# Kernel optimization log

Hardware: AMD Instinct MI355X
Metric: run time of the kernel (lower is better)

The kernel has to match this reference:

```python
import jax, jax.numpy as jnp
import numpy as np

T, D = 1024, 2048
H, KH, HD = 16, 4, 128
E, K, I = 8, 2, 2048
EPS = 1e-5
CAP = 30.0          # attn logit softcap and router logit softcap
BASE = 10000.0      # rope theta


def setup_inputs() -> dict:
    key = jax.random.key(0)
    ks = jax.random.split(key, 8)
    s = 0.02
    return {
        "positions": jnp.arange(T, dtype=jnp.int32),
        "hidden_states": jax.random.normal(ks[0], (T, D), jnp.float32),
        "w_qkv": jax.random.normal(ks[1], (D, (H + 2 * KH) * HD), jnp.float32) * s,
        "w_o": jax.random.normal(ks[2], (H * HD, D), jnp.float32) * s,
        "w_gate": jax.random.normal(ks[3], (D, E), jnp.float32) * s,
        "w_gate_up": jax.random.normal(ks[4], (E, D, 2 * I), jnp.float32) * s,
        "w_down": jax.random.normal(ks[5], (E, I, D), jnp.float32) * s,
        "w_pre_attn": 1.0 + 0.01 * jax.random.normal(ks[6], (D,), jnp.float32),
        "w_post_attn": jnp.ones((D,), jnp.float32),
        "w_pre_moe": 1.0 + 0.01 * jax.random.normal(ks[7], (D,), jnp.float32),
        "w_post_moe": jnp.ones((D,), jnp.float32),
    }


def rmsnorm(x, w):
    v = jnp.mean(jnp.square(x), axis=-1, keepdims=True)
    return x * jax.lax.rsqrt(v + EPS) * w


def rope_neox(pos, x):
    # x: [T, nH, HD]; full-head-dim neox-style rotation
    half = HD // 2
    inv = 1.0 / (BASE ** (jnp.arange(half, dtype=jnp.float32) * 2.0 / HD))
    f = pos.astype(jnp.float32)[:, None] * inv            # [T, half]
    cos, sin = jnp.cos(f)[:, None, :], jnp.sin(f)[:, None, :]
    x1, x2 = x[..., :half], x[..., half:]
    return jnp.concatenate([x1 * cos - x2 * sin, x2 * cos + x1 * sin], axis=-1)


def attention(pos, x, w_qkv, w_o):
    qkv = x @ w_qkv
    q, k, v = jnp.split(qkv, [H * HD, (H + KH) * HD], axis=-1)
    q = rope_neox(pos, q.reshape(T, H, HD))
    k = rope_neox(pos, k.reshape(T, KH, HD))
    v = v.reshape(T, KH, HD)
    rep = H // KH                                          # GQA repeat
    k = jnp.repeat(k, rep, axis=1)
    v = jnp.repeat(v, rep, axis=1)
    s = jnp.einsum('qhd,khd->hqk', q, k) * (HD ** -0.5)
    s = CAP * jnp.tanh(s / CAP)                            # tanh logit cap
    causal = pos[:, None] >= pos[None, :]
    s = jnp.where(causal[None], s, -1e30)
    p = jax.nn.softmax(s, axis=-1)
    o = jnp.einsum('hqk,khd->qhd', p, v).reshape(T, H * HD)
    return o @ w_o


def moe(x, w_gate, w_gate_up, w_down):
    logits = x @ w_gate
    logits = CAP * jnp.tanh(logits / CAP)                  # router softcap
    probs = jax.nn.softmax(logits, axis=-1)
    topv, topi = jax.lax.top_k(probs, K)                   # no renorm (Grok1)
    comb = jnp.zeros((T, E), probs.dtype).at[jnp.arange(T)[:, None], topi].set(topv)
    gu = jnp.einsum('td,edf->etf', x, w_gate_up)           # [E,T,2I]
    g, u = jnp.split(gu, 2, axis=-1)
    act = jax.nn.gelu(g, approximate=True) * u             # GeluAndMul(tanh)
    out_e = jnp.einsum('eti,eid->etd', act, w_down)        # [E,T,D]
    return jnp.einsum('etd,te->td', out_e, comb)


def reference(positions, hidden_states, w_qkv, w_o, w_gate, w_gate_up, w_down,
              w_pre_attn, w_post_attn, w_pre_moe, w_post_moe):
    resid = hidden_states
    h = rmsnorm(hidden_states, w_pre_attn)
    a = attention(positions, h, w_qkv, w_o)
    resid = resid + rmsnorm(a, w_post_attn)                # post_attn_norm + add
    h = rmsnorm(resid, w_pre_moe)
    m = moe(h, w_gate, w_gate_up, w_down)
    return resid + rmsnorm(m, w_post_moe)
```

## Files before the change

### kernel.cpp

```cpp
#include <hip/hip_runtime.h>

#define TT 1024
#define DD 2048
#define NH 16
#define NKV 4
#define HDIM 128
#define NE 8
#define NI 2048
#define EPSF 1e-5f
#define NP 4

typedef short bf16x8 __attribute__((ext_vector_type(8)));
typedef float f32x4 __attribute__((ext_vector_type(4)));

__device__ __forceinline__ unsigned short f2bf(float x) {
  unsigned u = __float_as_uint(x);
  u += 0x7FFFu + ((u >> 16) & 1u);
  return (unsigned short)(u >> 16);
}
__device__ __forceinline__ float bf2f(unsigned short h) {
  return __uint_as_float((unsigned)h << 16);
}
__device__ __forceinline__ void split2(float a, unsigned short& h,
                                       unsigned short& l) {
  h = f2bf(a);
  l = f2bf(a - bf2f(h));
}
__device__ __forceinline__ float tanh_cap30(float v) {
  float e = __expf(v * (2.f / 30.f));
  return 30.f - 60.f / (e + 1.f);
}

__device__ __forceinline__ float wave_sum(float v) {
#pragma unroll
  for (int m = 32; m >= 1; m >>= 1) v += __shfl_xor(v, m, 64);
  return v;
}

__device__ __forceinline__ int swz4(int r) { return (r ^ (r >> 2)) & 3; }
__device__ __forceinline__ int swz8(int r) { return (r ^ (r >> 3)) & 7; }

__device__ __forceinline__ int swzoff(int row, int k) {
  return (k & ~31) | ((((k >> 3) & 3) ^ swz4(row & 15)) << 3) | (k & 7);
}

__device__ __forceinline__ void stage_gll(const unsigned short* src, int ld,
                                          char* ldsbase, int wid, int lane) {
#pragma unroll
  for (int j = 0; j < 2; ++j) {
    int idx = (wid * 2 + j) * 64 + lane;
    int r = idx >> 2, c = idx & 3;
    const unsigned short* g = src + (long)r * ld + c * 8;
    __builtin_amdgcn_global_load_lds(
        (const __attribute__((address_space(1))) unsigned int*)g,
        (__attribute__((address_space(3))) unsigned int*)(ldsbase +
                                                         (wid * 2 + j) * 1024),
        16, 0, 0);
  }
}
__device__ __forceinline__ void ld_frag(const char* base, int wrow, int l15,
                                        int lg, bf16x8* dst) {
#pragma unroll
  for (int i = 0; i < 4; ++i) {
    int row = wrow + i * 16 + l15;
    dst[i] = *(const bf16x8*)(base + row * 64 + ((lg ^ swz4(row)) << 4));
  }
}
__device__ __forceinline__ void mm16(const bf16x8* xa, const bf16x8* xb,
                                     f32x4 (*acc)[4]) {
#pragma unroll
  for (int mi = 0; mi < 4; ++mi)
#pragma unroll
    for (int ni = 0; ni < 4; ++ni)
      acc[mi][ni] = __builtin_amdgcn_mfma_f32_16x16x32_bf16(
          xa[mi], xb[ni], acc[mi][ni], 0, 0, 0);
}

template <int MODE>
__global__ __launch_bounds__(256) void pgemm3_k(
    const unsigned short* __restrict__ Ah, const unsigned short* __restrict__ Al,
    const unsigned short* __restrict__ Bh, const unsigned short* __restrict__ Bl,
    float* __restrict__ C, int Kh, int lda, int ldb, int ldc, long czs,
    float escale, float* __restrict__ SM, float* __restrict__ SS,
    const float* __restrict__ Sf) {
  int z = blockIdx.z;
  int m0 = blockIdx.y * 128, n0 = blockIdx.x * 128;
  int k0 = 0, kend = Kh;
  const float* Sbase = nullptr;
  int head = 0;
  if (MODE == 0) {
    k0 = z * Kh;
    kend = k0 + Kh;
    C += (long)z * czs;
  } else if (MODE == 1) {
    if (blockIdx.x > blockIdx.y) return;
    Ah += (long)z * TT * lda;
    Al += (long)z * TT * lda;
    Bh += (long)(z >> 2) * TT * ldb;
    Bl += (long)(z >> 2) * TT * ldb;
    C += (long)z * czs;
  } else {
    head = z >> 3;
    int ch = z & 7;
    int limit = (blockIdx.y + 1) * 128;
    k0 = ch * 128;
    if (k0 >= limit) return;
    kend = k0 + 128;
    Sbase = Sf + (long)head * TT * TT;
    Bh += (long)(head >> 2) * HDIM * ldb;
    Bl += (long)(head >> 2) * HDIM * ldb;
    C += (long)ch * czs + head * HDIM;
  }

  __shared__ __align__(16) char lds[32768];
  __shared__ float mrow[128], invrow[128];
  int tid = threadIdx.x, lane = tid & 63, wid = tid >> 6;
  int wm = (wid >> 1) * 64, wn = (wid & 1) * 64;
  int l15 = lane & 15, lg = lane >> 4;

  if (MODE == 2) {
    if (tid < 128) {
      int q = m0 + tid;
      int nt = blockIdx.y + 1;
      float m = -1e30f;
      for (int t = 0; t < nt; ++t)
        m = fmaxf(m, SM[((long)head * 8 + t) * TT + q]);
      float den = 0.f;
      for (int t = 0; t < nt; ++t) {
        long so = ((long)head * 8 + t) * TT + q;
        den += SS[so] * __expf(SM[so] - m);
      }
      mrow[tid] = m;
      invrow[tid] = 1.f / den;
    }
  }

  f32x4 acc[4][4];
#pragma unroll
  for (int i = 0; i < 4; ++i)
#pragma unroll
    for (int j = 0; j < 4; ++j) acc[i][j] = {0.f, 0.f, 0.f, 0.f};

  for (int kt = k0; kt < kend; kt += 32) {
    __syncthreads();
    if (MODE == 2) {
#pragma unroll
      for (int j = 0; j < 2; ++j) {
        int idx = tid + j * 256;
        int r = idx >> 2, c = idx & 3;
        int q = m0 + r;
        const float* sp = Sbase + (long)q * TT + kt + c * 8;
        float4 s0 = *(const float4*)sp;
        float4 s1 = *(const float4*)(sp + 4);
        float mq = mrow[r], iq = invrow[r];
        bf16x8 ph, pl;
        int kg0 = kt + c * 8;
#pragma unroll
        for (int u = 0; u < 8; ++u) {
          float s = (u < 4) ? ((const float*)&s0)[u] : ((const float*)&s1)[u - 4];
          float p = (kg0 + u <= q) ? __expf(s - mq) * iq : 0.f;
          unsigned short hh, ll;
          split2(p, hh, ll);
          ((unsigned short*)&ph)[u] = hh;
          ((unsigned short*)&pl)[u] = ll;
        }
        int off = r * 64 + ((c ^ swz4(r)) << 4);
        *(bf16x8*)(lds + off) = ph;
        *(bf16x8*)(lds + 8192 + off) = pl;
      }
    } else {
      stage_gll(Ah + (long)m0 * lda + kt, lda, lds, wid, lane);
      stage_gll(Al + (long)m0 * lda + kt, lda, lds + 8192, wid, lane);
    }
    stage_gll(Bh + (long)n0 * ldb + kt, ldb, lds + 16384, wid, lane);
    stage_gll(Bl + (long)n0 * ldb + kt, ldb, lds + 24576, wid, lane);
    __syncthreads();
    bf16x8 fah[4], fal[4], fbh[4], fbl[4];
    ld_frag(lds, wm, l15, lg, fah);
    ld_frag(lds + 16384, wn, l15, lg, fbh);
    mm16(fah, fbh, acc);
    ld_frag(lds + 24576, wn, l15, lg, fbl);
    mm16(fah, fbl, acc);
    ld_frag(lds + 8192, wm, l15, lg, fal);
    mm16(fal, fbh, acc);
  }

  if (MODE == 1) {
    int bx = blockIdx.x;
    bool diag = (bx == blockIdx.y);
    float vcap[4][4][4];
#pragma unroll
    for (int mi = 0; mi < 4; ++mi)
#pragma unroll
      for (int ni = 0; ni < 4; ++ni)
#pragma unroll
        for (int rr = 0; rr < 4; ++rr)
          vcap[mi][ni][rr] = tanh_cap30(acc[mi][ni][rr] * escale);
#pragma unroll
    for (int mi = 0; mi < 4; ++mi)
#pragma unroll
      for (int ni = 0; ni < 4; ++ni)
#pragma unroll
        for (int rr = 0; rr < 4; ++rr) {
          int ml = m0 + wm + mi * 16 + lg * 4 + rr;
          int col = n0 + wn + ni * 16 + l15;
          C[(long)ml * ldc + col] = vcap[mi][ni][rr];
        }
    __syncthreads();
    float* wmx = (float*)lds;
    float* wsm = (float*)(lds + 1024);
    int ch = wid & 1;
#pragma unroll
    for (int mi = 0; mi < 4; ++mi)
#pragma unroll
      for (int rr = 0; rr < 4; ++rr) {
        int wr = wm + mi * 16 + lg * 4 + rr;
        int rowg = m0 + wr;
        float mx = -1e30f;
#pragma unroll
        for (int ni = 0; ni < 4; ++ni) {
          int colg = n0 + wn + ni * 16 + l15;
          if (!diag || colg <= rowg) mx = fmaxf(mx, vcap[mi][ni][rr]);
        }
#pragma unroll
        for (int mk = 1; mk <= 8; mk <<= 1)
          mx = fmaxf(mx, __shfl_xor(mx, mk, 64));
        if (l15 == 0) wmx[ch * 128 + wr] = mx;
      }
    __syncthreads();
#pragma unroll
    for (int mi = 0; mi < 4; ++mi)
#pragma unroll
      for (int rr = 0; rr < 4; ++rr) {
        int wr = wm + mi * 16 + lg * 4 + rr;
        int rowg = m0 + wr;
        float m2 = fmaxf(wmx[wr], wmx[128 + wr]);
        float s = 0.f;
#pragma unroll
        for (int ni = 0; ni < 4; ++ni) {
          int colg = n0 + wn + ni * 16 + l15;
          if (!diag || colg <= rowg) s += __expf(vcap[mi][ni][rr] - m2);
        }
#pragma unroll
        for (int mk = 1; mk <= 8; mk <<= 1) s += __shfl_xor(s, mk, 64);
        if (l15 == 0) wsm[ch * 128 + wr] = s;
      }
    __syncthreads();
    if (tid < 128) {
      float m2 = fmaxf(wmx[tid], wmx[128 + tid]);
      float s = wsm[tid] + wsm[128 + tid];
      long so = ((long)z * 8 + bx) * TT + m0 + tid;
      SM[so] = m2;
      SS[so] = s;
    }
    return;
  }

#pragma unroll
  for (int mi = 0; mi < 4; ++mi)
#pragma unroll
    for (int ni = 0; ni < 4; ++ni)
#pragma unroll
      for (int rr = 0; rr < 4; ++rr) {
        int ml = m0 + wm + mi * 16 + lg * 4 + rr;
        int col = n0 + wn + ni * 16 + l15;
        C[(long)ml * ldc + col] = acc[mi][ni][rr];
      }
}

template <int AMODE, int EP>
__global__ __launch_bounds__(256) void gemm_k(
    const unsigned short* __restrict__ A, const float* __restrict__ Bf,
    unsigned short* __restrict__ Cb, int N, int K, int lda, int ldb, int ldc,
    long bzs, long pzs, const int* __restrict__ cnt,
    const int* __restrict__ basep, const int* __restrict__ tok,
    const int* __restrict__ slotp, const float* __restrict__ wtp,
    unsigned short* __restrict__ slots_out) {
  int z = blockIdx.z;
  int e = z >> 1, kp = z & 1;
  Bf += (long)e * bzs;
  int Me = cnt[e], be = basep[e];
  int m0 = blockIdx.y * 128, n0 = blockIdx.x * 128;
  if (m0 >= Me) return;
  int Kc = K >> 1, kbeg = kp * Kc, klim = kbeg + Kc;

  __shared__ __align__(16) char lds[32768];
  const int BOFF = 16384;
  int tid = threadIdx.x, lane = tid & 63, wid = tid >> 6;
  int wm = (wid >> 1) * 64, wn = (wid & 1) * 64;
  int l15 = lane & 15, lg = lane >> 4;

  f32x4 acc[4][4];
#pragma unroll
  for (int i = 0; i < 4; ++i)
#pragma unroll
    for (int j = 0; j < 4; ++j) acc[i][j] = {0.f, 0.f, 0.f, 0.f};

  for (int kt = kbeg; kt < klim; kt += 64) {
    __syncthreads();
#pragma unroll
    for (int i = 0; i < 4; ++i) {
      int idx = (wid * 4 + i) * 64 + lane;
      int r = idx >> 3, c = idx & 7;
      int gm = m0 + r;
      long arow;
      if (AMODE == 1)
        arow = (gm < Me) ? (long)tok[e * TT + gm] : 0;
      else
        arow = (long)be + gm;
      int cs = c ^ swz8(r);
      const unsigned short* g = A + arow * (long)lda + kt + cs * 8;
      __builtin_amdgcn_global_load_lds(
          (const __attribute__((address_space(1))) unsigned int*)g,
          (__attribute__((address_space(3))) unsigned int*)(lds +
                                                           (wid * 4 + i) * 1024),
          16, 0, 0);
    }
#pragma unroll
    for (int i = 0; i < 4; ++i) {
      int gidx = tid + i * 256;
      int n = gidx & 127, kc = gidx >> 7;
      const float* src = Bf + (long)(kt + kc * 8) * ldb + n0 + n;
      bf16x8 v;
#pragma unroll
      for (int u = 0; u < 8; ++u)
        ((unsigned short*)&v)[u] = f2bf(src[(long)u * ldb]);
      *(bf16x8*)(lds + BOFF + n * 128 + ((kc ^ swz8(n)) << 4)) = v;
    }
    __syncthreads();
#pragma unroll
    for (int s = 0; s < 2; ++s) {
      bf16x8 af[4], bfr[4];
      int slotk = s * 4 + lg;
#pragma unroll
      for (int mi = 0; mi < 4; ++mi) {
        int row = wm + mi * 16 + l15;
        af[mi] =
            *(const bf16x8*)(lds + row * 128 + ((slotk ^ swz8(row)) << 4));
      }
#pragma unroll
      for (int ni = 0; ni < 4; ++ni) {
        int row = wn + ni * 16 + l15;
        bfr[ni] = *(const bf16x8*)(lds + BOFF + row * 128 +
                                   ((slotk ^ swz8(row)) << 4));
      }
      mm16(af, bfr, acc);
    }
  }
#pragma unroll
  for (int mi = 0; mi < 4; ++mi)
#pragma unroll
    for (int ni = 0; ni < 4; ++ni)
#pragma unroll
      for (int rr = 0; rr < 4; ++rr) {
        int ml = m0 + wm + mi * 16 + lg * 4 + rr;
        int col = n0 + wn + ni * 16 + l15;
        float val = acc[mi][ni][rr];
        if (ml < Me) {
          if (EP == 0) {
            Cb[(long)kp * pzs + (long)(be + ml) * ldc + col] = f2bf(val);
          } else {
            int t = tok[e * TT + ml];
            int s = slotp[e * TT + ml];
            float w = wtp[e * TT + ml];
            slots_out[(long)kp * pzs + ((long)s * TT + t) * DD + col] =
                f2bf(val * w);
          }
        }
      }
}

__global__ __launch_bounds__(256) void tsplit2_k(
    const float* __restrict__ Wq, unsigned short* __restrict__ Thq,
    unsigned short* __restrict__ Tlq, const float* __restrict__ Wo,
    unsigned short* __restrict__ Tho, unsigned short* __restrict__ Tlo) {
  __shared__ float lds[64 * 65];
  int b = blockIdx.x;
  const float* W;
  unsigned short *Th, *Tl;
  int K = DD, N, bx, by;
  if (b < 1536) {
    W = Wq; Th = Thq; Tl = Tlq; N = 3072; bx = b % 48; by = b / 48;
  } else {
    int b2 = b - 1536;
    W = Wo; Th = Tho; Tl = Tlo; N = DD; bx = b2 % 32; by = b2 / 32;
  }
  int n0 = bx * 64, k0 = by * 64;
  int tid = threadIdx.x;
#pragma unroll
  for (int i = 0; i < 4; ++i) {
    int idx = tid + i * 256;
    int kr = idx >> 4, cg = idx & 15;
    float4 v = *(const float4*)(W + (long)(k0 + kr) * N + n0 + cg * 4);
    float* p = &lds[kr * 65 + cg * 4];
    p[0] = v.x; p[1] = v.y; p[2] = v.z; p[3] = v.w;
  }
  __syncthreads();
#pragma unroll
  for (int i = 0; i < 2; ++i) {
    int idx = tid + i * 256;
    int n = idx >> 3, kc = idx & 7;
    bf16x8 h8, l8;
#pragma unroll
    for (int u = 0; u < 8; ++u) {
      unsigned short hh, ll;
      split2(lds[(kc * 8 + u) * 65 + n], hh, ll);
      ((unsigned short*)&h8)[u] = hh;
      ((unsigned short*)&l8)[u] = ll;
    }
    int row = n0 + n;
    long o = (long)row * K + swzoff(row, k0 + kc * 8);
    *(bf16x8*)(Th + o) = h8;
    *(bf16x8*)(Tl + o) = l8;
  }
}

__global__ __launch_bounds__(256) void rms_pre_k(const float* __restrict__ x,
                                                 const float* __restrict__ w,
                                                 unsigned short* __restrict__ oh,
                                                 unsigned short* __restrict__ ol) {
  __shared__ float red[4];
  int t = blockIdx.x, tid = threadIdx.x;
  const float* xr = x + (long)t * DD;
  float xv[8];
  float ss = 0.f;
#pragma unroll
  for (int i = 0; i < 8; ++i) {
    float v = xr[tid + i * 256];
    xv[i] = v;
    ss += v * v;
  }
  ss = wave_sum(ss);
  if ((tid & 63) == 0) red[tid >> 6] = ss;
  __syncthreads();
  float r = rsqrtf((red[0] + red[1] + red[2] + red[3]) * (1.f / DD) + EPSF);
#pragma unroll
  for (int i = 0; i < 8; ++i) {
    int d = tid + i * 256;
    int ds = swzoff(t, d);
    split2(xv[i] * r * w[d], oh[(long)t * DD + ds], ol[(long)t * DD + ds]);
  }
}

__global__ __launch_bounds__(256) void ropevt_k(
    const int* __restrict__ pos, const float* __restrict__ qp,
    unsigned short* __restrict__ qh, unsigned short* __restrict__ ql,
    unsigned short* __restrict__ kh, unsigned short* __restrict__ kl,
    unsigned short* __restrict__ Vh, unsigned short* __restrict__ Vl) {
  __shared__ __align__(16) float smem[64 * 129];
  int b = blockIdx.x, tid = threadIdx.x;
  const long PS = (long)TT * 3072;
  if (b < TT) {
    float* cs = smem;
    float* sn = smem + 64;
    int t = b;
    float pf = (float)pos[t];
    if (tid < 64) {
      float inv = exp2f(-(float)tid * 0.20762050593046015f);
      float f = pf * inv;
      cs[tid] = cosf(f);
      sn[tid] = sinf(f);
    }
    __syncthreads();
    const float* row = qp + (long)t * 3072;
#pragma unroll
    for (int i = 0; i < 4; ++i) {
      int idx = tid + i * 256;
      int h = idx >> 6, j = idx & 63;
      float x1 = 0.f, x2 = 0.f;
#pragma unroll
      for (int p = 0; p < NP; ++p) {
        x1 += row[p * PS + h * HDIM + j];
        x2 += row[p * PS + h * HDIM + 64 + j];
      }
      float c = cs[j], s = sn[j];
      long base = ((long)h * TT + t) * HDIM;
      split2(x1 * c - x2 * s, qh[base + swzoff(t, j)], ql[base + swzoff(t, j)]);
      split2(x2 * c + x1 * s, qh[base + swzoff(t, 64 + j)],
             ql[base + swzoff(t, 64 + j)]);
    }
    {
      int k2 = tid >> 6, j = tid & 63;
      float x1 = 0.f, x2 = 0.f;
#pragma unroll
      for (int p = 0; p < NP; ++p) {
        x1 += row[p * PS + 2048 + k2 * HDIM + j];
        x2 += row[p * PS + 2048 + k2 * HDIM + 64 + j];
      }
      float c = cs[j], s = sn[j];
      long base = ((long)k2 * TT + t) * HDIM;
      split2(x1 * c - x2 * s, kh[base + swzoff(t, j)], kl[base + swzoff(t, j)]);
      split2(x2 * c + x1 * s, kh[base + swzoff(t, 64 + j)],
             kl[base + swzoff(t, 64 + j)]);
    }
  } else {
    int bb = b - TT;
    int tb = bb & 7, kv = bb >> 3;
    int t0 = tb * 128;
#pragma unroll
    for (int dh = 0; dh < 2; ++dh) {
      if (dh) __syncthreads();
#pragma unroll
      for (int i = 0; i < 8; ++i) {
        int fidx = tid + i * 256;
        int t = fidx >> 4, dq = fidx & 15;
        long gi = (long)(t0 + t) * 3072 + 2560 + kv * HDIM + dh * 64 + dq * 4;
        float4 a = *(const float4*)(qp + gi);
#pragma unroll
        for (int p = 1; p < NP; ++p) {
          float4 bb4 = *(const float4*)(qp + p * PS + gi);
          a.x += bb4.x; a.y += bb4.y; a.z += bb4.z; a.w += bb4.w;
        }
        smem[(dq * 4 + 0) * 129 + t] = a.x;
        smem[(dq * 4 + 1) * 129 + t] = a.y;
        smem[(dq * 4 + 2) * 129 + t] = a.z;
        smem[(dq * 4 + 3) * 129 + t] = a.w;
      }
      __syncthreads();
#pragma unroll
      for (int i = 0; i < 4; ++i) {
        int cidx = tid + i * 256;
        int d = cidx >> 4, tc = cidx & 15;
        bf16x8 h8, l8;
#pragma unroll
        for (int u = 0; u < 8; ++u) {
          unsigned short hh, ll;
          split2(smem[d * 129 + tc * 8 + u], hh, ll);
          ((unsigned short*)&h8)[u] = hh;
          ((unsigned short*)&l8)[u] = ll;
        }
        int rowd = dh * 64 + d;
        long o = ((long)kv * HDIM + rowd) * TT + swzoff(rowd, t0 + tc * 8);
        *(bf16x8*)(Vh + o) = h8;
        *(bf16x8*)(Vl + o) = l8;
      }
    }
  }
}

__global__ __launch_bounds__(256) void obreduce_k(const float* __restrict__ obp,
                                                  unsigned short* __restrict__ oh,
                                                  unsigned short* __restrict__ ol) {
  int m = blockIdx.x, tid = threadIdx.x;
  int nv = (m >> 7) + 1;
#pragma unroll
  for (int i = 0; i < 8; ++i) {
    int d = tid + i * 256;
    float s = 0.f;
    for (int c = 0; c < nv; ++c) s += obp[(long)c * TT * DD + (long)m * DD + d];
    int ds = swzoff(m, d);
    split2(s, oh[(long)m * DD + ds], ol[(long)m * DD + ds]);
  }
}

__global__ __launch_bounds__(256) void post_attn_gate_k(
    const float* __restrict__ ap, const float* __restrict__ hidden,
    const float* __restrict__ w_post, const float* __restrict__ w_pre2,
    const float* __restrict__ wg, float* __restrict__ resid1,
    unsigned short* __restrict__ h2b, int* cnt, int* tok, int* slotp,
    float* wtp) {
  __shared__ float red[4];
  __shared__ float red8[4][8];
  int t = blockIdx.x, tid = threadIdx.x;
  const long PS = (long)TT * DD;
  float av[8];
  float ss = 0.f;
#pragma unroll
  for (int i = 0; i < 8; ++i) {
    long o = (long)t * DD + tid + i * 256;
    float v = 0.f;
#pragma unroll
    for (int p = 0; p < NP; ++p) v += ap[p * PS + o];
    av[i] = v;
    ss += v * v;
  }
  ss = wave_sum(ss);
  if ((tid & 63) == 0) red[tid >> 6] = ss;
  __syncthreads();
  float r1 = rsqrtf((red[0] + red[1] + red[2] + red[3]) * (1.f / DD) + EPSF);
  __syncthreads();
  float rv[8];
  float ss2 = 0.f;
#pragma unroll
  for (int i = 0; i < 8; ++i) {
    int d = tid + i * 256;
    float v = hidden[(long)t * DD + d] + av[i] * r1 * w_post[d];
    rv[i] = v;
    resid1[(long)t * DD + d] = v;
    ss2 += v * v;
  }
  ss2 = wave_sum(ss2);
  if ((tid & 63) == 0) red[tid >> 6] = ss2;
  __syncthreads();
  float r2 = rsqrtf((red[0] + red[1] + red[2] + red[3]) * (1.f / DD) + EPSF);
  float a[8] = {0, 0, 0, 0, 0, 0, 0, 0};
#pragma unroll
  for (int i = 0; i < 8; ++i) {
    int d = tid + i * 256;
    float hv = rv[i] * r2 * w_pre2[d];
    h2b[(long)t * DD + d] = f2bf(hv);
    const float* wr = wg + d * 8;
#pragma unroll
    for (int e = 0; e < 8; ++e) a[e] += hv * wr[e];
  }
#pragma unroll
  for (int e = 0; e < 8; ++e) a[e] = wave_sum(a[e]);
  if ((tid & 63) == 0) {
#pragma unroll
    for (int e = 0; e < 8; ++e) red8[tid >> 6][e] = a[e];
  }
  __syncthreads();
  if (tid == 0) {
    float l[8], p[8];
    float m = -1e30f;
    for (int e = 0; e < 8; ++e) {
      float v = red8[0][e] + red8[1][e] + red8[2][e] + red8[3][e];
      v = 30.f * tanhf(v * (1.f / 30.f));
      l[e] = v;
      m = fmaxf(m, v);
    }
    float s = 0.f;
    for (int e = 0; e < 8; ++e) { p[e] = expf(l[e] - m); s += p[e]; }
    for (int e = 0; e < 8; ++e) p[e] /= s;
    int i1 = 0;
    for (int e = 1; e < 8; ++e) if (p[e] > p[i1]) i1 = e;
    int i2 = (i1 == 0) ? 1 : 0;
    for (int e = 0; e < 8; ++e) if (e != i1 && p[e] > p[i2]) i2 = e;
    int q1 = atomicAdd(&cnt[i1], 1);
    tok[i1 * TT + q1] = t; slotp[i1 * TT + q1] = 0; wtp[i1 * TT + q1] = p[i1];
    int q2 = atomicAdd(&cnt[i2], 1);
    tok[i2 * TT + q2] = t; slotp[i2 * TT + q2] = 1; wtp[i2 * TT + q2] = p[i2];
  }
}

__global__ void scan_k(const int* __restrict__ cnt, int* __restrict__ basep) {
  if (threadIdx.x == 0) {
    int s = 0;
    for (int e = 0; e < NE; ++e) { basep[e] = s; s += cnt[e]; }
    basep[NE] = s;
  }
}

__global__ __launch_bounds__(256) void act_k(const unsigned short* __restrict__ gu,
                                             unsigned short* __restrict__ actb) {
  long a = blockIdx.x;
  const long PS = (long)2 * TT * 2 * NI;
  const unsigned short* g0 = gu + a * (2 * NI);
  const unsigned short* g1 = g0 + PS;
  for (int i = threadIdx.x; i < NI; i += 256) {
    float gg = bf2f(g0[i]) + bf2f(g1[i]);
    float uu = bf2f(g0[i + NI]) + bf2f(g1[i + NI]);
    float y = 0.7978845608028654f * (gg + 0.044715f * gg * gg * gg);
    float ey = __expf(2.f * y);
    float th = 1.f - 2.f / (ey + 1.f);
    actb[a * NI + i] = f2bf(0.5f * gg * (1.f + th) * uu);
  }
}

__global__ __launch_bounds__(256) void final_k(
    const float* __restrict__ resid1, const unsigned short* __restrict__ slots,
    const float* __restrict__ w2, float* __restrict__ out) {
  __shared__ float red[4];
  int t = blockIdx.x, tid = threadIdx.x;
  const long PL = (long)TT * DD;
  float mv[8];
  float ss = 0.f;
#pragma unroll
  for (int i = 0; i < 8; ++i) {
    long o = (long)t * DD + tid + i * 256;
    float v = bf2f(slots[o]) + bf2f(slots[PL + o]) + bf2f(slots[2 * PL + o]) +
              bf2f(slots[3 * PL + o]);
    mv[i] = v;
    ss += v * v;
  }
  ss = wave_sum(ss);
  if ((tid & 63) == 0) red[tid >> 6] = ss;
  __syncthreads();
  float r = rsqrtf((red[0] + red[1] + red[2] + red[3]) * (1.f / DD) + EPSF);
#pragma unroll
  for (int i = 0; i < 8; ++i) {
    int d = tid + i * 256;
    out[(long)t * DD + d] = resid1[(long)t * DD + d] + mv[i] * r * w2[d];
  }
}

__global__ void sentinel_k(float* out) { out[threadIdx.x] = 12345.0f; }

extern "C" void kernel_launch(void* const* d_in, const int* in_sizes, int n_in,
                              void* d_out, int out_size, void* d_ws,
                              size_t ws_size, hipStream_t stream) {
  const int* pos = (const int*)d_in[0];
  const float* hidden = (const float*)d_in[1];
  const float* w_qkv = (const float*)d_in[2];
  const float* w_o = (const float*)d_in[3];
  const float* w_gate = (const float*)d_in[4];
  const float* w_gu = (const float*)d_in[5];
  const float* w_down = (const float*)d_in[6];
  const float* w_pre_attn = (const float*)d_in[7];
  const float* w_post_attn = (const float*)d_in[8];
  const float* w_pre_moe = (const float*)d_in[9];
  const float* w_post_moe = (const float*)d_in[10];
  float* out = (float*)d_out;

  char* ws = (char*)d_ws;
  size_t off = 0;
  auto alloc = [&](size_t bytes) {
    char* p = ws + off;
    off += (bytes + 255) & ~(size_t)255;
    return p;
  };
  typedef unsigned short u16;
  u16* h1h = (u16*)alloc((size_t)TT * DD * 2);
  u16* h1l = (u16*)alloc((size_t)TT * DD * 2);
  u16* wqkvTh = (u16*)alloc((size_t)3072 * DD * 2);
  u16* wqkvTl = (u16*)alloc((size_t)3072 * DD * 2);
  float* qkvp = (float*)alloc((size_t)NP * TT * 3072 * 4);
  u16* qh_ = (u16*)alloc((size_t)NH * TT * HDIM * 2);
  u16* ql_ = (u16*)alloc((size_t)NH * TT * HDIM * 2);
  u16* kh_ = (u16*)alloc((size_t)NKV * TT * HDIM * 2);
  u16* kl_ = (u16*)alloc((size_t)NKV * TT * HDIM * 2);
  u16* vth = (u16*)alloc((size_t)NKV * HDIM * TT * 2);
  u16* vtl = (u16*)alloc((size_t)NKV * HDIM * TT * 2);
  float* S = (float*)alloc((size_t)NH * TT * TT * 4);
  float* SMb = (float*)alloc((size_t)NH * 8 * TT * 4);
  float* SSb = (float*)alloc((size_t)NH * 8 * TT * 4);
  float* obp = (float*)alloc((size_t)8 * TT * DD * 4);
  u16* obh = (u16*)alloc((size_t)TT * DD * 2);
  u16* obl = (u16*)alloc((size_t)TT * DD * 2);
  u16* woTh = (u16*)alloc((size_t)DD * DD * 2);
  u16* woTl = (u16*)alloc((size_t)DD * DD * 2);
  float* attnp = (float*)alloc((size_t)NP * TT * DD * 4);
  float* resid1 = (float*)alloc((size_t)TT * DD * 4);
  u16* h2b = (u16*)alloc((size_t)TT * DD * 2);
  int* cnt = (int*)alloc(NE * 4);
  int* basep = (int*)alloc((NE + 1) * 4);
  int* tok = (int*)alloc((size_t)NE * TT * 4);
  int* slotp = (int*)alloc((size_t)NE * TT * 4);
  float* wtp = (float*)alloc((size_t)NE * TT * 4);
  u16* gu = (u16*)alloc((size_t)2 * 2 * TT * 2 * NI * 2);
  u16* actb = (u16*)alloc((size_t)2 * TT * NI * 2);
  u16* slots = (u16*)alloc((size_t)2 * 2 * TT * DD * 2);

  if (off > ws_size) {
    sentinel_k<<<1, 256, 0, stream>>>(out);
    return;
  }

  hipMemsetAsync(cnt, 0, NE * 4, stream);
  dim3 blk(256);

  rms_pre_k<<<TT, blk, 0, stream>>>(hidden, w_pre_attn, h1h, h1l);
  tsplit2_k<<<2560, blk, 0, stream>>>(w_qkv, wqkvTh, wqkvTl, w_o, woTh, woTl);

  pgemm3_k<0><<<dim3(3072 / 128, TT / 128, NP), blk, 0, stream>>>(
      h1h, h1l, wqkvTh, wqkvTl, qkvp, DD / NP, DD, DD, 3072, (long)TT * 3072,
      0.f, nullptr, nullptr, nullptr);

  ropevt_k<<<TT + 32, blk, 0, stream>>>(pos, qkvp, qh_, ql_, kh_, kl_, vth,
                                        vtl);

  pgemm3_k<1><<<dim3(TT / 128, TT / 128, NH), blk, 0, stream>>>(
      qh_, ql_, kh_, kl_, S, HDIM, HDIM, HDIM, TT, (long)TT * TT,
      0.08838834764831845f, SMb, SSb, nullptr);

  pgemm3_k<2><<<dim3(1, TT / 128, NH * 8), blk, 0, stream>>>(
      nullptr, nullptr, vth, vtl, obp, 128, TT, TT, DD, (long)TT * DD, 0.f,
      SMb, SSb, S);
  obreduce_k<<<TT, blk, 0, stream>>>(obp, obh, obl);

  pgemm3_k<0><<<dim3(DD / 128, TT / 128, NP), blk, 0, stream>>>(
      obh, obl, woTh, woTl, attnp, DD / NP, DD, DD, DD, (long)TT * DD, 0.f,
      nullptr, nullptr, nullptr);

  post_attn_gate_k<<<TT, blk, 0, stream>>>(attnp, hidden, w_post_attn,
                                           w_pre_moe, w_gate, resid1, h2b, cnt,
                                           tok, slotp, wtp);
  scan_k<<<1, 64, 0, stream>>>(cnt, basep);

  gemm_k<1, 0><<<dim3(2 * NI / 128, TT / 128, NE * 2), blk, 0, stream>>>(
      h2b, w_gu, gu, 2 * NI, DD, DD, 2 * NI, 2 * NI, (long)DD * 2 * NI,
      (long)2 * TT * 2 * NI, cnt, basep, tok, nullptr, nullptr, nullptr);

  act_k<<<2 * TT, blk, 0, stream>>>(gu, actb);

  gemm_k<2, 3><<<dim3(DD / 128, TT / 128, NE * 2), blk, 0, stream>>>(
      actb, w_down, nullptr, DD, NI, NI, DD, DD, (long)NI * DD,
      (long)2 * TT * DD, cnt, basep, tok, slotp, wtp, slots);

  final_k<<<TT, blk, 0, stream>>>(resid1, slots, w_post_moe, out);
}
```

Measured before the change: 455.0 us.

## Split MoE GEMMs four ways along K and fold prep kernels together

The MoE gate-up and down GEMMs move from a 2-way to a 4-way K split, doubling the grid z-dimension so more blocks run when each expert only has a few token tiles. The activation and final kernels now sum four bf16 partials per slot (eight in the final kernel) instead of two or four. The pre-attention RMSNorm and the counter reset are folded into the weight transpose/split kernel, and the scan kernel is dropped in favour of each GEMM block computing its expert base inline. This saves several launches and a memset in exchange for more partial-sum traffic and extra bf16 rounding of the partials.

New measurement: 478.0 us. 5.1% more time.

```diff
diff --git a/kernel.cpp b/kernel.cpp
--- a/kernel.cpp
+++ b/kernel.cpp
@@ -268,21 +268,22 @@
       }
 }
 
-template <int AMODE, int EP>
+template <int AMODE, int EP, int KSL>
 __global__ __launch_bounds__(256) void gemm_k(
     const unsigned short* __restrict__ A, const float* __restrict__ Bf,
     unsigned short* __restrict__ Cb, int N, int K, int lda, int ldb, int ldc,
     long bzs, long pzs, const int* __restrict__ cnt,
-    const int* __restrict__ basep, const int* __restrict__ tok,
-    const int* __restrict__ slotp, const float* __restrict__ wtp,
-    unsigned short* __restrict__ slots_out) {
+    const int* __restrict__ tok, const int* __restrict__ slotp,
+    const float* __restrict__ wtp, unsigned short* __restrict__ slots_out) {
   int z = blockIdx.z;
-  int e = z >> 1, kp = z & 1;
+  int e = z >> KSL, kp = z & ((1 << KSL) - 1);
   Bf += (long)e * bzs;
-  int Me = cnt[e], be = basep[e];
+  int Me = cnt[e];
+  int be = 0;
+  for (int q = 0; q < e; ++q) be += cnt[q];
   int m0 = blockIdx.y * 128, n0 = blockIdx.x * 128;
   if (m0 >= Me) return;
-  int Kc = K >> 1, kbeg = kp * Kc, klim = kbeg + Kc;
+  int Kc = K >> KSL, kbeg = kp * Kc, klim = kbeg + Kc;
 
   __shared__ __align__(16) char lds[32768];
   const int BOFF = 16384;
@@ -370,12 +371,40 @@
       }
 }
 
-__global__ __launch_bounds__(256) void tsplit2_k(
+__global__ __launch_bounds__(256) void prep_k(
     const float* __restrict__ Wq, unsigned short* __restrict__ Thq,
     unsigned short* __restrict__ Tlq, const float* __restrict__ Wo,
-    unsigned short* __restrict__ Tho, unsigned short* __restrict__ Tlo) {
+    unsigned short* __restrict__ Tho, unsigned short* __restrict__ Tlo,
+    const float* __restrict__ x, const float* __restrict__ wpre,
+    unsigned short* __restrict__ h1h, unsigned short* __restrict__ h1l,
+    int* __restrict__ cnt) {
   __shared__ float lds[64 * 65];
-  int b = blockIdx.x;
+  int b = blockIdx.x, tid = threadIdx.x;
+  if (b == 0 && tid < NE) cnt[tid] = 0;
+  if (b >= 2560) {
+    int t = b - 2560;
+    const float* xr = x + (long)t * DD;
+    float xv[8];
+    float ss = 0.f;
+#pragma unroll
+    for (int i = 0; i < 8; ++i) {
+      float v = xr[tid + i * 256];
+      xv[i] = v;
+      ss += v * v;
+    }
+    ss = wave_sum(ss);
+    if ((tid & 63) == 0) lds[tid >> 6] = ss;
+    __syncthreads();
+    float r = rsqrtf((lds[0] + lds[1] + lds[2] + lds[3]) * (1.f / DD) + EPSF);
+#pragma unroll
+    for (int i = 0; i < 8; ++i) {
+      int d = tid + i * 256;
+      int ds = swzoff(t, d);
+      split2(xv[i] * r * wpre[d], h1h[(long)t * DD + ds],
+             h1l[(long)t * DD + ds]);
+    }
+    return;
+  }
   const float* W;
   unsigned short *Th, *Tl;
   int K = DD, N, bx, by;
@@ -386,7 +415,6 @@
     W = Wo; Th = Tho; Tl = Tlo; N = DD; bx = b2 % 32; by = b2 / 32;
   }
   int n0 = bx * 64, k0 = by * 64;
-  int tid = threadIdx.x;
 #pragma unroll
   for (int i = 0; i < 4; ++i) {
     int idx = tid + i * 256;
@@ -412,33 +440,6 @@
     long o = (long)row * K + swzoff(row, k0 + kc * 8);
     *(bf16x8*)(Th + o) = h8;
     *(bf16x8*)(Tl + o) = l8;
-  }
-}
-
-__global__ __launch_bounds__(256) void rms_pre_k(const float* __restrict__ x,
-                                                 const float* __restrict__ w,
-                                                 unsigned short* __restrict__ oh,
-                                                 unsigned short* __restrict__ ol) {
-  __shared__ float red[4];
-  int t = blockIdx.x, tid = threadIdx.x;
-  const float* xr = x + (long)t * DD;
-  float xv[8];
-  float ss = 0.f;
-#pragma unroll
-  for (int i = 0; i < 8; ++i) {
-    float v = xr[tid + i * 256];
-    xv[i] = v;
-    ss += v * v;
-  }
-  ss = wave_sum(ss);
-  if ((tid & 63) == 0) red[tid >> 6] = ss;
-  __syncthreads();
-  float r = rsqrtf((red[0] + red[1] + red[2] + red[3]) * (1.f / DD) + EPSF);
-#pragma unroll
-  for (int i = 0; i < 8; ++i) {
-    int d = tid + i * 256;
-    int ds = swzoff(t, d);
-    split2(xv[i] * r * w[d], oh[(long)t * DD + ds], ol[(long)t * DD + ds]);
   }
 }
 
@@ -633,23 +634,18 @@
   }
 }
 
-__global__ void scan_k(const int* __restrict__ cnt, int* __restrict__ basep) {
-  if (threadIdx.x == 0) {
-    int s = 0;
-    for (int e = 0; e < NE; ++e) { basep[e] = s; s += cnt[e]; }
-    basep[NE] = s;
-  }
-}
-
 __global__ __launch_bounds__(256) void act_k(const unsigned short* __restrict__ gu,
                                              unsigned short* __restrict__ actb) {
   long a = blockIdx.x;
   const long PS = (long)2 * TT * 2 * NI;
   const unsigned short* g0 = gu + a * (2 * NI);
-  const unsigned short* g1 = g0 + PS;
   for (int i = threadIdx.x; i < NI; i += 256) {
-    float gg = bf2f(g0[i]) + bf2f(g1[i]);
-    float uu = bf2f(g0[i + NI]) + bf2f(g1[i + NI]);
+    float gg = 0.f, uu = 0.f;
+#pragma unroll
+    for (int p = 0; p < 4; ++p) {
+      gg += bf2f(g0[p * PS + i]);
+      uu += bf2f(g0[p * PS + i + NI]);
+    }
     float y = 0.7978845608028654f * (gg + 0.044715f * gg * gg * gg);
     float ey = __expf(2.f * y);
     float th = 1.f - 2.f / (ey + 1.f);
@@ -668,8 +664,9 @@
 #pragma unroll
   for (int i = 0; i < 8; ++i) {
     long o = (long)t * DD + tid + i * 256;
-    float v = bf2f(slots[o]) + bf2f(slots[PL + o]) + bf2f(slots[2 * PL + o]) +
-              bf2f(slots[3 * PL + o]);
+    float v = 0.f;
+#pragma unroll
+    for (int p = 0; p < 8; ++p) v += bf2f(slots[p * PL + o]);
     mv[i] = v;
     ss += v * v;
   }
@@ -733,24 +730,23 @@
   float* resid1 = (float*)alloc((size_t)TT * DD * 4);
   u16* h2b = (u16*)alloc((size_t)TT * DD * 2);
   int* cnt = (int*)alloc(NE * 4);
-  int* basep = (int*)alloc((NE + 1) * 4);
   int* tok = (int*)alloc((size_t)NE * TT * 4);
   int* slotp = (int*)alloc((size_t)NE * TT * 4);
   float* wtp = (float*)alloc((size_t)NE * TT * 4);
-  u16* gu = (u16*)alloc((size_t)2 * 2 * TT * 2 * NI * 2);
+  u16* gu = (u16*)alloc((size_t)4 * 2 * TT * 2 * NI * 2);
   u16* actb = (u16*)alloc((size_t)2 * TT * NI * 2);
-  u16* slots = (u16*)alloc((size_t)2 * 2 * TT * DD * 2);
+  u16* slots = (u16*)alloc((size_t)4 * 2 * TT * DD * 2);
 
   if (off > ws_size) {
     sentinel_k<<<1, 256, 0, stream>>>(out);
     return;
   }
 
-  hipMemsetAsync(cnt, 0, NE * 4, stream);
   dim3 blk(256);
 
-  rms_pre_k<<<TT, blk, 0, stream>>>(hidden, w_pre_attn, h1h, h1l);
-  tsplit2_k<<<2560, blk, 0, stream>>>(w_qkv, wqkvTh, wqkvTl, w_o, woTh, woTl);
+  prep_k<<<2560 + TT, blk, 0, stream>>>(w_qkv, wqkvTh, wqkvTl, w_o, woTh,
+                                        woTl, hidden, w_pre_attn, h1h, h1l,
+                                        cnt);
 
   pgemm3_k<0><<<dim3(3072 / 128, TT / 128, NP), blk, 0, stream>>>(
       h1h, h1l, wqkvTh, wqkvTl, qkvp, DD / NP, DD, DD, 3072, (long)TT * 3072,
@@ -775,17 +771,16 @@
   post_attn_gate_k<<<TT, blk, 0, stream>>>(attnp, hidden, w_post_attn,
                                            w_pre_moe, w_gate, resid1, h2b, cnt,
                                            tok, slotp, wtp);
-  scan_k<<<1, 64, 0, stream>>>(cnt, basep);
-
-  gemm_k<1, 0><<<dim3(2 * NI / 128, TT / 128, NE * 2), blk, 0, stream>>>(
+
+  gemm_k<1, 0, 2><<<dim3(2 * NI / 128, TT / 128, NE * 4), blk, 0, stream>>>(
       h2b, w_gu, gu, 2 * NI, DD, DD, 2 * NI, 2 * NI, (long)DD * 2 * NI,
-      (long)2 * TT * 2 * NI, cnt, basep, tok, nullptr, nullptr, nullptr);
+      (long)2 * TT * 2 * NI, cnt, tok, nullptr, nullptr, nullptr);
 
   act_k<<<2 * TT, blk, 0, stream>>>(gu, actb);
 
-  gemm_k<2, 3><<<dim3(DD / 128, TT / 128, NE * 2), blk, 0, stream>>>(
+  gemm_k<2, 3, 2><<<dim3(DD / 128, TT / 128, NE * 4), blk, 0, stream>>>(
       actb, w_down, nullptr, DD, NI, NI, DD, DD, (long)NI * DD,
-      (long)2 * TT * DD, cnt, basep, tok, slotp, wtp, slots);
+      (long)2 * TT * DD, cnt, tok, slotp, wtp, slots);
 
   final_k<<<TT, blk, 0, stream>>>(resid1, slots, w_post_moe, out);
 }
```
